# Optimization experiments

Hardware: AMD Instinct MI355X
Metric: run time of the kernel (lower is better)

Reference implementation:

```python
import jax, jax.numpy as jnp
import numpy as np

L = 1024
D = 512      # d_model
H = 256      # hidden


def setup_inputs() -> dict:
    key = jax.random.key(0)
    k1, k2, k3, k4, k5 = jax.random.split(key, 5)
    scale = 0.02
    return {
        "seq_feats": jax.random.normal(k1, (L, D), dtype=jnp.float32),
        "W1": jax.random.normal(k2, (H, 2 * D), dtype=jnp.float32) * scale,
        "b1": jax.random.normal(k3, (H,), dtype=jnp.float32) * scale,
        "W2": jax.random.normal(k4, (1, H), dtype=jnp.float32) * scale,
        "b2": jax.random.normal(k5, (1,), dtype=jnp.float32) * scale,
    }


def reference(seq_feats, W1, b1, W2, b2):
    # cat([a, b]) @ W1.T == a @ W1[:, :D].T + b @ W1[:, D:].T
    # so we never materialize the [L, L, 2D] concat tensor.
    d = seq_feats.shape[1]
    pa = seq_feats @ W1[:, :d].T          # [L, H] (row / i contribution)
    pb = seq_feats @ W1[:, d:].T          # [L, H] (col / j contribution)
    h = jax.nn.relu(pa[:, None, :] + pb[None, :, :] + b1)  # [L, L, H]
    scores = jnp.einsum("ijh,h->ij", h, W2[0]) + b2[0]      # [L, L]
    scores = (scores + scores.T) * 0.5
    return jax.nn.sigmoid(scores)
```

## Files before the change

kernel.cpp:

```cpp
#include <hip/hip_runtime.h>
#include <math.h>

#define LL 1024
#define DD 512
#define HH 256


__global__ __launch_bounds__(512) void sp_gemm(
    const float* __restrict__ S, const float* __restrict__ W1,
    const float* __restrict__ b1, float* __restrict__ O) {
  __shared__ float Sl[2][64][36];
  __shared__ float Wl[2][32][36];

  const int tid = threadIdx.x;
  const int tx  = tid & 15;
  const int ty  = tid >> 4;
  const int i0  = blockIdx.x * 64;
  const int n0  = blockIdx.y * 32;

  const int srow = tid >> 3;
  const int sc   = tid & 7;
  const int wn   = n0 + ((tid >> 3) & 31);
  const float* sp = S  + (size_t)(i0 + srow) * DD + 4 * sc;
  const float* wp = W1 + (size_t)(wn & 255) * (2 * DD) + (wn >> 8) * DD + 4 * sc;

  float4 sreg, wreg;
  auto ld = [&](int c) {
    sreg = *(const float4*)(sp + 32 * c);
    if (tid < 256) wreg = *(const float4*)(wp + 32 * c);
  };
  auto st = [&](int b) {
    *(float4*)&Sl[b][srow][4 * sc] = sreg;
    if (tid < 256) *(float4*)&Wl[b][tid >> 3][4 * sc] = wreg;
  };

  float acc[2][2] = {{0.f}};

  ld(0); st(0); __syncthreads();

  for (int c = 0; c < 16; ++c) {
    const int cur = c & 1;
    if (c < 15) ld(c + 1);
    #pragma unroll
    for (int k4 = 0; k4 < 8; ++k4) {
      const float4 wf0 = *(const float4*)&Wl[cur][tx][4 * k4];
      const float4 wf1 = *(const float4*)&Wl[cur][tx + 16][4 * k4];
      const float4 sf0 = *(const float4*)&Sl[cur][2 * ty][4 * k4];
      const float4 sf1 = *(const float4*)&Sl[cur][2 * ty + 1][4 * k4];
      acc[0][0] += sf0.x * wf0.x + sf0.y * wf0.y + sf0.z * wf0.z + sf0.w * wf0.w;
      acc[0][1] += sf0.x * wf1.x + sf0.y * wf1.y + sf0.z * wf1.z + sf0.w * wf1.w;
      acc[1][0] += sf1.x * wf0.x + sf1.y * wf0.y + sf1.z * wf0.z + sf1.w * wf0.w;
      acc[1][1] += sf1.x * wf1.x + sf1.y * wf1.y + sf1.z * wf1.z + sf1.w * wf1.w;
    }
    if (c < 15) st(cur ^ 1);
    __syncthreads();
  }

  #pragma unroll
  for (int b = 0; b < 2; ++b) {
    const int n = n0 + tx + 16 * b;
    const float bb = (n < 256) ? b1[n] : 0.f;
    float2 v = make_float2(acc[0][b] + bb, acc[1][b] + bb);
    *(float2*)(O + (size_t)n * LL + i0 + 2 * ty) = v;
  }
}

__global__ __launch_bounds__(1024) void sp_pairwise(
    const float* __restrict__ O, const float* __restrict__ W2,
    float* __restrict__ sraw) {
  __shared__ float Tl[HH][72];
  __shared__ float Ul[HH][72];
  __shared__ float PA[8][128];
  __shared__ float As[64], Bs[64];

  const int tid = threadIdx.x;
  const int tx  = tid & 31;
  const int ty  = tid >> 5;
  const int i0  = blockIdx.y * 64;
  const int j0  = blockIdx.x * 64;

  #pragma unroll
  for (int q = 0; q < 4; ++q) {
    const int m = q * 1024 + tid;
    const int h = m >> 4, g = m & 15;
    *(float4*)&Tl[h][4 * g] = *(const float4*)(O + (size_t)h * LL + i0 + 4 * g);
    *(float4*)&Ul[h][4 * g] = *(const float4*)(O + (size_t)(HH + h) * LL + j0 + 4 * g);
  }
  __syncthreads();

  {
    const int x = tid & 127, hs = tid >> 7;
    const float* pan = (x < 64) ? &Tl[0][x] : &Ul[0][x - 64];
    float p = 0.f;
    #pragma unroll 8
    for (int n = 0; n < 32; ++n) {
      const int h = hs * 32 + n;
      p = fmaf(pan[h * 72], W2[h], p);
    }
    PA[hs][x] = p;
  }
  __syncthreads();
  if (tid < 128) {
    float s = 0.f;
    #pragma unroll
    for (int q = 0; q < 8; ++q) s += PA[q][tid];
    if (tid < 64) As[tid] = s; else Bs[tid - 64] = s;
  }
  __syncthreads();

  float a00 = 0.f, a01 = 0.f, a10 = 0.f, a11 = 0.f;

  #pragma unroll 4
  for (int h = 0; h < HH; ++h) {
    const float2 tv = *(const float2*)&Tl[h][2 * ty];
    const float2 uv = *(const float2*)&Ul[h][2 * tx];
    const float w = W2[h];
    a00 = fmaf(fabsf(tv.x + uv.x), w, a00);
    a01 = fmaf(fabsf(tv.x + uv.y), w, a01);
    a10 = fmaf(fabsf(tv.y + uv.x), w, a10);
    a11 = fmaf(fabsf(tv.y + uv.y), w, a11);
  }

  const float A0 = As[2 * ty], A1 = As[2 * ty + 1];
  const float B0 = Bs[2 * tx], B1 = Bs[2 * tx + 1];
  float* p0 = sraw + (size_t)(i0 + 2 * ty) * LL + j0 + 2 * tx;
  *(float2*)p0        = make_float2(a00 + A0 + B0, a01 + A0 + B1);
  *(float2*)(p0 + LL) = make_float2(a10 + A1 + B0, a11 + A1 + B1);
}

__global__ __launch_bounds__(1024) void sp_symsig(
    const float* __restrict__ sraw, const float* __restrict__ b2,
    float* __restrict__ out) {
  __shared__ float B[64][65];
  const int i0 = blockIdx.y * 64;
  const int j0 = blockIdx.x * 64;
  const int r  = threadIdx.x >> 4;
  const int g  = threadIdx.x & 15;

  const float4 bt = *(const float4*)(sraw + (size_t)(j0 + r) * LL + i0 + 4 * g);
  B[r][4 * g + 0] = bt.x;
  B[r][4 * g + 1] = bt.y;
  B[r][4 * g + 2] = bt.z;
  B[r][4 * g + 3] = bt.w;
  __syncthreads();

  const float4 a = *(const float4*)(sraw + (size_t)(i0 + r) * LL + j0 + 4 * g);
  const float bb = b2[0];
  float4 o;
  float x;
  x = 0.25f * (a.x + B[4 * g + 0][r]) + bb; o.x = 1.f / (1.f + expf(-x));
  x = 0.25f * (a.y + B[4 * g + 1][r]) + bb; o.y = 1.f / (1.f + expf(-x));
  x = 0.25f * (a.z + B[4 * g + 2][r]) + bb; o.z = 1.f / (1.f + expf(-x));
  x = 0.25f * (a.w + B[4 * g + 3][r]) + bb; o.w = 1.f / (1.f + expf(-x));
  *(float4*)(out + (size_t)(i0 + r) * LL + j0 + 4 * g) = o;
}

extern "C" void kernel_launch(void* const* d_in, const int* in_sizes, int n_in,
                              void* d_out, int out_size, void* d_ws, size_t ws_size,
                              hipStream_t stream) {
  const float* S  = (const float*)d_in[0];
  const float* W1 = (const float*)d_in[1];
  const float* b1 = (const float*)d_in[2];
  const float* W2 = (const float*)d_in[3];
  const float* b2 = (const float*)d_in[4];
  float* out = (float*)d_out;

  float* ws   = (float*)d_ws;
  float* O    = ws;
  float* sraw = ws + 512 * LL;

  hipLaunchKernelGGL(sp_gemm, dim3(16, 16), dim3(512), 0, stream,
                     S, W1, b1, O);
  hipLaunchKernelGGL(sp_pairwise, dim3(16, 16), dim3(1024), 0, stream,
                     O, W2, sraw);
  hipLaunchKernelGGL(sp_symsig, dim3(16, 16), dim3(1024), 0, stream,
                     sraw, b2, out);
}
```

Before: 49.93 us.

## Split-K the projection GEMM and enlarge per-thread tiles in GEMM and pairwise

The projection GEMM now uses 128x64 output tiles with a 4x4 register tile per thread and splits the K dimension four ways across blockIdx.z, writing four partial buffers. The pairwise kernel sums those partials and adds b1 while loading them into shared memory. It also runs 256 threads that each compute a 4x4 tile instead of 1024 threads computing 2x2 tiles, which gives more register reuse of shared-memory loads. The cost is extra workspace, extra global traffic to read back the four partials in every pairwise block, and fewer threads per pairwise block.

```diff
diff --git a/kernel.cpp b/kernel.cpp
--- a/kernel.cpp
+++ b/kernel.cpp
@@ -8,83 +8,111 @@
 
 __global__ __launch_bounds__(512) void sp_gemm(
     const float* __restrict__ S, const float* __restrict__ W1,
-    const float* __restrict__ b1, float* __restrict__ O) {
-  __shared__ float Sl[2][64][36];
-  __shared__ float Wl[2][32][36];
+    float* __restrict__ pC) {
+  __shared__ float Sl[2][128][36];
+  __shared__ float Wl[2][64][36];
 
   const int tid = threadIdx.x;
   const int tx  = tid & 15;
   const int ty  = tid >> 4;
-  const int i0  = blockIdx.x * 64;
-  const int n0  = blockIdx.y * 32;
+  const int i0  = blockIdx.x * 128;
+  const int n0  = blockIdx.y * 64;
+  const int kz  = blockIdx.z * 128;
 
   const int srow = tid >> 3;
-  const int sc   = tid & 7;
-  const int wn   = n0 + ((tid >> 3) & 31);
-  const float* sp = S  + (size_t)(i0 + srow) * DD + 4 * sc;
-  const float* wp = W1 + (size_t)(wn & 255) * (2 * DD) + (wn >> 8) * DD + 4 * sc;
-
-  float4 sreg, wreg;
+  const int ssl  = tid & 7;
+  const int wn   = n0 + srow;
+  const float* s0 = S + (size_t)(i0 + srow) * DD + kz + 4 * ssl;
+  const float* s1 = S + (size_t)(i0 + 64 + srow) * DD + kz + 4 * ssl;
+  const float* w0 = W1 + (size_t)(wn & 255) * (2 * DD) + (wn >> 8) * DD + kz + 4 * ssl;
+
+  float4 sA, sB, wA;
   auto ld = [&](int c) {
-    sreg = *(const float4*)(sp + 32 * c);
-    if (tid < 256) wreg = *(const float4*)(wp + 32 * c);
+    sA = *(const float4*)(s0 + 32 * c);
+    sB = *(const float4*)(s1 + 32 * c);
+    wA = *(const float4*)(w0 + 32 * c);
   };
   auto st = [&](int b) {
-    *(float4*)&Sl[b][srow][4 * sc] = sreg;
-    if (tid < 256) *(float4*)&Wl[b][tid >> 3][4 * sc] = wreg;
+    *(float4*)&Sl[b][srow][4 * ssl]      = sA;
+    *(float4*)&Sl[b][64 + srow][4 * ssl] = sB;
+    *(float4*)&Wl[b][srow][4 * ssl]      = wA;
   };
 
-  float acc[2][2] = {{0.f}};
+  float acc[4][4] = {{0.f}};
 
   ld(0); st(0); __syncthreads();
 
-  for (int c = 0; c < 16; ++c) {
+  for (int c = 0; c < 4; ++c) {
     const int cur = c & 1;
-    if (c < 15) ld(c + 1);
-    #pragma unroll
+    if (c < 3) ld(c + 1);
+    #pragma unroll 2
     for (int k4 = 0; k4 < 8; ++k4) {
-      const float4 wf0 = *(const float4*)&Wl[cur][tx][4 * k4];
-      const float4 wf1 = *(const float4*)&Wl[cur][tx + 16][4 * k4];
-      const float4 sf0 = *(const float4*)&Sl[cur][2 * ty][4 * k4];
-      const float4 sf1 = *(const float4*)&Sl[cur][2 * ty + 1][4 * k4];
-      acc[0][0] += sf0.x * wf0.x + sf0.y * wf0.y + sf0.z * wf0.z + sf0.w * wf0.w;
-      acc[0][1] += sf0.x * wf1.x + sf0.y * wf1.y + sf0.z * wf1.z + sf0.w * wf1.w;
-      acc[1][0] += sf1.x * wf0.x + sf1.y * wf0.y + sf1.z * wf0.z + sf1.w * wf0.w;
-      acc[1][1] += sf1.x * wf1.x + sf1.y * wf1.y + sf1.z * wf1.z + sf1.w * wf1.w;
+      float4 wf[4], sf[4];
+      #pragma unroll
+      for (int b = 0; b < 4; ++b) wf[b] = *(const float4*)&Wl[cur][tx + 16 * b][4 * k4];
+      #pragma unroll
+      for (int a = 0; a < 4; ++a) sf[a] = *(const float4*)&Sl[cur][4 * ty + a][4 * k4];
+      #pragma unroll
+      for (int a = 0; a < 4; ++a) {
+        #pragma unroll
+        for (int b = 0; b < 4; ++b) {
+          acc[a][b] += sf[a].x * wf[b].x + sf[a].y * wf[b].y +
+                       sf[a].z * wf[b].z + sf[a].w * wf[b].w;
+        }
+      }
     }
-    if (c < 15) st(cur ^ 1);
+    if (c < 3) st(cur ^ 1);
     __syncthreads();
   }
 
+  float* base = pC + (size_t)blockIdx.z * (512 * LL);
   #pragma unroll
-  for (int b = 0; b < 2; ++b) {
+  for (int b = 0; b < 4; ++b) {
     const int n = n0 + tx + 16 * b;
-    const float bb = (n < 256) ? b1[n] : 0.f;
-    float2 v = make_float2(acc[0][b] + bb, acc[1][b] + bb);
-    *(float2*)(O + (size_t)n * LL + i0 + 2 * ty) = v;
-  }
-}
-
-__global__ __launch_bounds__(1024) void sp_pairwise(
-    const float* __restrict__ O, const float* __restrict__ W2,
-    float* __restrict__ sraw) {
+    *(float4*)(base + (size_t)n * LL + i0 + 4 * ty) =
+        make_float4(acc[0][b], acc[1][b], acc[2][b], acc[3][b]);
+  }
+}
+
+__global__ __launch_bounds__(256) void sp_pairwise(
+    const float* __restrict__ pC, const float* __restrict__ b1,
+    const float* __restrict__ W2, float* __restrict__ sraw) {
   __shared__ float Tl[HH][72];
   __shared__ float Ul[HH][72];
-  __shared__ float PA[8][128];
+  __shared__ float PR[2][128];
   __shared__ float As[64], Bs[64];
 
   const int tid = threadIdx.x;
-  const int tx  = tid & 31;
-  const int ty  = tid >> 5;
+  const int tx  = tid & 15;
+  const int ty  = tid >> 4;
   const int i0  = blockIdx.y * 64;
   const int j0  = blockIdx.x * 64;
-
-  #pragma unroll
-  for (int q = 0; q < 4; ++q) {
-    const int m = q * 1024 + tid;
-    const int h = m >> 4, g = m & 15;
-    *(float4*)&Tl[h][4 * g] = *(const float4*)(O + (size_t)h * LL + i0 + 4 * g);
-    *(float4*)&Ul[h][4 * g] = *(const float4*)(O + (size_t)(HH + h) * LL + j0 + 4 * g);
+  const size_t PZ = 512 * (size_t)LL;
+
+  #pragma unroll 2
+  for (int q = 0; q < 16; ++q) {
+    const int m = q * 256 + tid;
+    const int h = m >> 4;
+    const int g4 = (m & 15) * 4;
+    const float* pt = pC + (size_t)h * LL + i0 + g4;
+    const float* pu = pC + (size_t)(HH + h) * LL + j0 + g4;
+    const float4 t0 = *(const float4*)(pt);
+    const float4 t1 = *(const float4*)(pt + PZ);
+    const float4 t2 = *(const float4*)(pt + 2 * PZ);
+    const float4 t3 = *(const float4*)(pt + 3 * PZ);
+    const float4 u0 = *(const float4*)(pu);
+    const float4 u1 = *(const float4*)(pu + PZ);
+    const float4 u2 = *(const float4*)(pu + 2 * PZ);
+    const float4 u3 = *(const float4*)(pu + 3 * PZ);
+    const float bb = b1[h];
+    *(float4*)&Tl[h][g4] = make_float4(t0.x + t1.x + t2.x + t3.x + bb,
+                                       t0.y + t1.y + t2.y + t3.y + bb,
+                                       t0.z + t1.z + t2.z + t3.z + bb,
+                                       t0.w + t1.w + t2.w + t3.w + bb);
+    *(float4*)&Ul[h][g4] = make_float4(u0.x + u1.x + u2.x + u3.x,
+                                       u0.y + u1.y + u2.y + u3.y,
+                                       u0.z + u1.z + u2.z + u3.z,
+                                       u0.w + u1.w + u2.w + u3.w);
   }
   __syncthreads();
 
@@ -93,39 +121,47 @@
     const float* pan = (x < 64) ? &Tl[0][x] : &Ul[0][x - 64];
     float p = 0.f;
     #pragma unroll 8
-    for (int n = 0; n < 32; ++n) {
-      const int h = hs * 32 + n;
+    for (int n = 0; n < 128; ++n) {
+      const int h = hs * 128 + n;
       p = fmaf(pan[h * 72], W2[h], p);
     }
-    PA[hs][x] = p;
+    PR[hs][x] = p;
   }
   __syncthreads();
   if (tid < 128) {
-    float s = 0.f;
-    #pragma unroll
-    for (int q = 0; q < 8; ++q) s += PA[q][tid];
+    const float s = PR[0][tid] + PR[1][tid];
     if (tid < 64) As[tid] = s; else Bs[tid - 64] = s;
   }
   __syncthreads();
 
-  float a00 = 0.f, a01 = 0.f, a10 = 0.f, a11 = 0.f;
+  float acc[4][4] = {{0.f}};
 
   #pragma unroll 4
   for (int h = 0; h < HH; ++h) {
-    const float2 tv = *(const float2*)&Tl[h][2 * ty];
-    const float2 uv = *(const float2*)&Ul[h][2 * tx];
+    const float4 tv4 = *(const float4*)&Tl[h][4 * ty];
+    const float4 uv4 = *(const float4*)&Ul[h][4 * tx];
     const float w = W2[h];
-    a00 = fmaf(fabsf(tv.x + uv.x), w, a00);
-    a01 = fmaf(fabsf(tv.x + uv.y), w, a01);
-    a10 = fmaf(fabsf(tv.y + uv.x), w, a10);
-    a11 = fmaf(fabsf(tv.y + uv.y), w, a11);
-  }
-
-  const float A0 = As[2 * ty], A1 = As[2 * ty + 1];
-  const float B0 = Bs[2 * tx], B1 = Bs[2 * tx + 1];
-  float* p0 = sraw + (size_t)(i0 + 2 * ty) * LL + j0 + 2 * tx;
-  *(float2*)p0        = make_float2(a00 + A0 + B0, a01 + A0 + B1);
-  *(float2*)(p0 + LL) = make_float2(a10 + A1 + B0, a11 + A1 + B1);
+    const float tv[4] = {tv4.x, tv4.y, tv4.z, tv4.w};
+    const float uv[4] = {uv4.x, uv4.y, uv4.z, uv4.w};
+    #pragma unroll
+    for (int a = 0; a < 4; ++a) {
+      #pragma unroll
+      for (int b = 0; b < 4; ++b) {
+        acc[a][b] = fmaf(fabsf(tv[a] + uv[b]), w, acc[a][b]);
+      }
+    }
+  }
+
+  #pragma unroll
+  for (int a = 0; a < 4; ++a) {
+    const float Ai = As[4 * ty + a];
+    float4 v;
+    v.x = acc[a][0] + Ai + Bs[4 * tx + 0];
+    v.y = acc[a][1] + Ai + Bs[4 * tx + 1];
+    v.z = acc[a][2] + Ai + Bs[4 * tx + 2];
+    v.w = acc[a][3] + Ai + Bs[4 * tx + 3];
+    *(float4*)(sraw + (size_t)(i0 + 4 * ty + a) * LL + j0 + 4 * tx) = v;
+  }
 }
 
 __global__ __launch_bounds__(1024) void sp_symsig(
@@ -166,13 +202,13 @@
   float* out = (float*)d_out;
 
   float* ws   = (float*)d_ws;
-  float* O    = ws;
-  float* sraw = ws + 512 * LL;
-
-  hipLaunchKernelGGL(sp_gemm, dim3(16, 16), dim3(512), 0, stream,
-                     S, W1, b1, O);
-  hipLaunchKernelGGL(sp_pairwise, dim3(16, 16), dim3(1024), 0, stream,
-                     O, W2, sraw);
+  float* pC   = ws;
+  float* sraw = ws + 4 * 512 * LL;
+
+  hipLaunchKernelGGL(sp_gemm, dim3(8, 8, 4), dim3(512), 0, stream,
+                     S, W1, pC);
+  hipLaunchKernelGGL(sp_pairwise, dim3(16, 16), dim3(256), 0, stream,
+                     pC, b1, W2, sraw);
   hipLaunchKernelGGL(sp_symsig, dim3(16, 16), dim3(1024), 0, stream,
                      sraw, b2, out);
 }
```

New measurement: 58.50 us. +17.2%, slower.

## Store projections in bf16, split pairwise over hidden halves with 4x4 register tiles

Applied to the files above, without the earlier changes.

The GEMM output projections are now stored as bf16 instead of fp32, halving their memory and LDS footprint. The pairwise kernel uses 256-thread blocks computing 4x4 outputs per thread, which gives more register reuse per LDS load. The hidden dimension is split across two z-blocks that write partial score planes, and the symmetrize/sigmoid kernel sums them. This raises parallelism and cuts LDS traffic, but adds bf16 rounding error and an extra 4MB partial-plane write and read.

```diff
diff --git a/kernel.cpp b/kernel.cpp
--- a/kernel.cpp
+++ b/kernel.cpp
@@ -1,4 +1,5 @@
 #include <hip/hip_runtime.h>
+#include <hip/hip_bf16.h>
 #include <math.h>
 
 #define LL 1024
@@ -6,9 +7,20 @@
 #define HH 256
 
 
+__device__ __forceinline__ ushort f2bf(float f) {
+  __hip_bfloat16 h = __float2bfloat16(f);
+  return *reinterpret_cast<ushort*>(&h);
+}
+__device__ __forceinline__ float bf_lo(unsigned int u) {
+  return __uint_as_float(u << 16);
+}
+__device__ __forceinline__ float bf_hi(unsigned int u) {
+  return __uint_as_float(u & 0xffff0000u);
+}
+
 __global__ __launch_bounds__(512) void sp_gemm(
     const float* __restrict__ S, const float* __restrict__ W1,
-    const float* __restrict__ b1, float* __restrict__ O) {
+    const float* __restrict__ b1, ushort* __restrict__ O) {
   __shared__ float Sl[2][64][36];
   __shared__ float Wl[2][32][36];
 
@@ -60,98 +72,119 @@
   for (int b = 0; b < 2; ++b) {
     const int n = n0 + tx + 16 * b;
     const float bb = (n < 256) ? b1[n] : 0.f;
-    float2 v = make_float2(acc[0][b] + bb, acc[1][b] + bb);
-    *(float2*)(O + (size_t)n * LL + i0 + 2 * ty) = v;
-  }
-}
-
-__global__ __launch_bounds__(1024) void sp_pairwise(
-    const float* __restrict__ O, const float* __restrict__ W2,
-    float* __restrict__ sraw) {
-  __shared__ float Tl[HH][72];
-  __shared__ float Ul[HH][72];
-  __shared__ float PA[8][128];
+    ushort2 v;
+    v.x = f2bf(acc[0][b] + bb);
+    v.y = f2bf(acc[1][b] + bb);
+    *(ushort2*)(O + (size_t)n * LL + i0 + 2 * ty) = v;
+  }
+}
+
+__global__ __launch_bounds__(256, 4) void sp_pairwise(
+    const ushort* __restrict__ O, const float* __restrict__ W2,
+    float* __restrict__ pz) {
+  __shared__ ushort Tl[128][72];
+  __shared__ ushort Ul[128][72];
+  __shared__ float PR[2][128];
   __shared__ float As[64], Bs[64];
 
   const int tid = threadIdx.x;
-  const int tx  = tid & 31;
-  const int ty  = tid >> 5;
+  const int tx  = tid & 15;
+  const int ty  = tid >> 4;
+  const int j0  = blockIdx.x * 64;
   const int i0  = blockIdx.y * 64;
-  const int j0  = blockIdx.x * 64;
+  const int hz  = blockIdx.z * 128;
 
   #pragma unroll
-  for (int q = 0; q < 4; ++q) {
-    const int m = q * 1024 + tid;
-    const int h = m >> 4, g = m & 15;
-    *(float4*)&Tl[h][4 * g] = *(const float4*)(O + (size_t)h * LL + i0 + 4 * g);
-    *(float4*)&Ul[h][4 * g] = *(const float4*)(O + (size_t)(HH + h) * LL + j0 + 4 * g);
+  for (int q = 0; q < 8; ++q) {
+    const int m = q * 256 + tid;
+    const int hh = m >> 4;
+    const int g8 = (m & 15) * 4;
+    *(ushort4*)&Tl[hh][g8] =
+        *(const ushort4*)(O + (size_t)(hz + hh) * LL + i0 + g8);
+    *(ushort4*)&Ul[hh][g8] =
+        *(const ushort4*)(O + (size_t)(HH + hz + hh) * LL + j0 + g8);
   }
   __syncthreads();
 
   {
     const int x = tid & 127, hs = tid >> 7;
-    const float* pan = (x < 64) ? &Tl[0][x] : &Ul[0][x - 64];
+    const ushort* pan = (x < 64) ? &Tl[0][x] : &Ul[0][x - 64];
     float p = 0.f;
     #pragma unroll 8
-    for (int n = 0; n < 32; ++n) {
-      const int h = hs * 32 + n;
-      p = fmaf(pan[h * 72], W2[h], p);
+    for (int n = 0; n < 64; ++n) {
+      const int hh = hs * 64 + n;
+      const float v = __uint_as_float(((unsigned int)pan[hh * 72]) << 16);
+      p = fmaf(v, W2[hz + hh], p);
     }
-    PA[hs][x] = p;
+    PR[hs][x] = p;
   }
   __syncthreads();
   if (tid < 128) {
-    float s = 0.f;
+    const float s = PR[0][tid] + PR[1][tid];
+    if (tid < 64) As[tid] = s; else Bs[tid - 64] = s;
+  }
+  __syncthreads();
+
+  float acc[4][4] = {{0.f}};
+
+  #pragma unroll 4
+  for (int hh = 0; hh < 128; ++hh) {
+    const uint2 tr = *(const uint2*)&Tl[hh][4 * ty];
+    const uint2 ur = *(const uint2*)&Ul[hh][4 * tx];
+    const float w = W2[hz + hh];
+    const float tv[4] = {bf_lo(tr.x), bf_hi(tr.x), bf_lo(tr.y), bf_hi(tr.y)};
+    const float uv[4] = {bf_lo(ur.x), bf_hi(ur.x), bf_lo(ur.y), bf_hi(ur.y)};
     #pragma unroll
-    for (int q = 0; q < 8; ++q) s += PA[q][tid];
-    if (tid < 64) As[tid] = s; else Bs[tid - 64] = s;
-  }
-  __syncthreads();
-
-  float a00 = 0.f, a01 = 0.f, a10 = 0.f, a11 = 0.f;
-
-  #pragma unroll 4
-  for (int h = 0; h < HH; ++h) {
-    const float2 tv = *(const float2*)&Tl[h][2 * ty];
-    const float2 uv = *(const float2*)&Ul[h][2 * tx];
-    const float w = W2[h];
-    a00 = fmaf(fabsf(tv.x + uv.x), w, a00);
-    a01 = fmaf(fabsf(tv.x + uv.y), w, a01);
-    a10 = fmaf(fabsf(tv.y + uv.x), w, a10);
-    a11 = fmaf(fabsf(tv.y + uv.y), w, a11);
-  }
-
-  const float A0 = As[2 * ty], A1 = As[2 * ty + 1];
-  const float B0 = Bs[2 * tx], B1 = Bs[2 * tx + 1];
-  float* p0 = sraw + (size_t)(i0 + 2 * ty) * LL + j0 + 2 * tx;
-  *(float2*)p0        = make_float2(a00 + A0 + B0, a01 + A0 + B1);
-  *(float2*)(p0 + LL) = make_float2(a10 + A1 + B0, a11 + A1 + B1);
+    for (int a = 0; a < 4; ++a) {
+      #pragma unroll
+      for (int b = 0; b < 4; ++b) {
+        acc[a][b] = fmaf(fabsf(tv[a] + uv[b]), w, acc[a][b]);
+      }
+    }
+  }
+
+  float* po = pz + (size_t)blockIdx.z * ((size_t)LL * LL);
+  #pragma unroll
+  for (int a = 0; a < 4; ++a) {
+    const float Ai = As[4 * ty + a];
+    float4 v;
+    v.x = acc[a][0] + Ai + Bs[4 * tx + 0];
+    v.y = acc[a][1] + Ai + Bs[4 * tx + 1];
+    v.z = acc[a][2] + Ai + Bs[4 * tx + 2];
+    v.w = acc[a][3] + Ai + Bs[4 * tx + 3];
+    *(float4*)(po + (size_t)(i0 + 4 * ty + a) * LL + j0 + 4 * tx) = v;
+  }
 }
 
 __global__ __launch_bounds__(1024) void sp_symsig(
-    const float* __restrict__ sraw, const float* __restrict__ b2,
+    const float* __restrict__ pz, const float* __restrict__ b2,
     float* __restrict__ out) {
   __shared__ float B[64][65];
   const int i0 = blockIdx.y * 64;
   const int j0 = blockIdx.x * 64;
   const int r  = threadIdx.x >> 4;
   const int g  = threadIdx.x & 15;
-
-  const float4 bt = *(const float4*)(sraw + (size_t)(j0 + r) * LL + i0 + 4 * g);
-  B[r][4 * g + 0] = bt.x;
-  B[r][4 * g + 1] = bt.y;
-  B[r][4 * g + 2] = bt.z;
-  B[r][4 * g + 3] = bt.w;
-  __syncthreads();
-
-  const float4 a = *(const float4*)(sraw + (size_t)(i0 + r) * LL + j0 + 4 * g);
+  const size_t L2 = (size_t)LL * LL;
+
+  const float* pm = pz + (size_t)(j0 + r) * LL + i0 + 4 * g;
+  const float4 m0 = *(const float4*)(pm);
+  const float4 m1 = *(const float4*)(pm + L2);
+  B[r][4 * g + 0] = m0.x + m1.x;
+  B[r][4 * g + 1] = m0.y + m1.y;
+  B[r][4 * g + 2] = m0.z + m1.z;
+  B[r][4 * g + 3] = m0.w + m1.w;
+  __syncthreads();
+
+  const float* pd = pz + (size_t)(i0 + r) * LL + j0 + 4 * g;
+  const float4 d0 = *(const float4*)(pd);
+  const float4 d1 = *(const float4*)(pd + L2);
   const float bb = b2[0];
   float4 o;
   float x;
-  x = 0.25f * (a.x + B[4 * g + 0][r]) + bb; o.x = 1.f / (1.f + expf(-x));
-  x = 0.25f * (a.y + B[4 * g + 1][r]) + bb; o.y = 1.f / (1.f + expf(-x));
-  x = 0.25f * (a.z + B[4 * g + 2][r]) + bb; o.z = 1.f / (1.f + expf(-x));
-  x = 0.25f * (a.w + B[4 * g + 3][r]) + bb; o.w = 1.f / (1.f + expf(-x));
+  x = 0.25f * (d0.x + d1.x + B[4 * g + 0][r]) + bb; o.x = 1.f / (1.f + expf(-x));
+  x = 0.25f * (d0.y + d1.y + B[4 * g + 1][r]) + bb; o.y = 1.f / (1.f + expf(-x));
+  x = 0.25f * (d0.z + d1.z + B[4 * g + 2][r]) + bb; o.z = 1.f / (1.f + expf(-x));
+  x = 0.25f * (d0.w + d1.w + B[4 * g + 3][r]) + bb; o.w = 1.f / (1.f + expf(-x));
   *(float4*)(out + (size_t)(i0 + r) * LL + j0 + 4 * g) = o;
 }
 
@@ -165,14 +198,14 @@
   const float* b2 = (const float*)d_in[4];
   float* out = (float*)d_out;
 
-  float* ws   = (float*)d_ws;
-  float* O    = ws;
-  float* sraw = ws + 512 * LL;
+  float* ws = (float*)d_ws;
+  ushort* O = (ushort*)ws;
+  float* pz = ws + 262144;
 
   hipLaunchKernelGGL(sp_gemm, dim3(16, 16), dim3(512), 0, stream,
                      S, W1, b1, O);
-  hipLaunchKernelGGL(sp_pairwise, dim3(16, 16), dim3(1024), 0, stream,
-                     O, W2, sraw);
+  hipLaunchKernelGGL(sp_pairwise, dim3(16, 16, 2), dim3(256), 0, stream,
+                     O, W2, pz);
   hipLaunchKernelGGL(sp_symsig, dim3(16, 16), dim3(1024), 0, stream,
-                     sraw, b2, out);
-}
+                     pz, b2, out);
+}
```

After: 51.74 us. 1.04x slower.
